# Optimization experiments

Hardware: AMD Instinct MI355X
Metric: run time of the kernel (lower is better)

## Reference

```python
import jax, jax.numpy as jnp
import numpy as np

BINS = 1000  # torch: int(max-min)*100; ~1000 for standardized randn data, fixed for jit


def _entropy(counts, n, width):
    # torch.histogram(density=True): probs = counts / (n * bin_width)
    probs = counts / (n * width)
    safe = jnp.where(probs > 0, probs, 1.0)
    return jnp.sum(jnp.where(probs > 0, -probs * jnp.log2(safe), 0.0))


def setup_inputs() -> dict:
    key = jax.random.key(0)
    k1, k2 = jax.random.split(key)
    x = jax.random.normal(k1, (1024, 64, 16, 16), dtype=jnp.float32)
    u = jax.random.uniform(k2, (1024, 64, 16, 16), dtype=jnp.float32)  # dropout noise
    return {"x": x, "u": u}


def reference(x, u):
    B = x.shape[0]
    temp = x.reshape(B, -1)              # [B, D]
    D = temp.shape[1]

    # corrcoef across rows (each row is a variable)
    tc = temp - temp.mean(axis=1, keepdims=True)
    cov = tc @ tc.T                      # [B, B]
    d = jnp.sqrt(jnp.diag(cov))
    corr = cov / (d[:, None] * d[None, :])
    factor1 = jnp.mean(jnp.abs(corr), axis=1)            # [B]

    # global standardization (torch.std default is unbiased, ddof=1)
    tnorm = (temp - temp.mean()) / jnp.std(temp, ddof=1)
    lo, hi = tnorm.min(), tnorm.max()
    width = (hi - lo) / BINS
    idx = jnp.clip(jnp.floor((tnorm - lo) / width).astype(jnp.int32), 0, BINS - 1)

    # per-row histograms via batched scatter-add; batch histogram = sum of rows
    row_counts = jax.vmap(lambda ii: jnp.zeros(BINS, jnp.float32).at[ii].add(1.0))(idx)  # [B, BINS]
    batch_counts = row_counts.sum(axis=0)

    batch_entropy = _entropy(batch_counts, B * D, width)
    local_entropy = jax.vmap(lambda c: _entropy(c, D, width))(row_counts)  # [B]

    f2 = local_entropy / batch_entropy
    is_zero = f2 == 0
    f1 = jnp.where(is_zero, 0.0, factor1)
    f2 = jnp.where(is_zero, 1.0, jnp.where(f2 < 1.0, 1.0 / f2, f2))
    keep = f1 / f2                       # 1 - p, per row
    p = 1.0 - keep                       # [B]

    mask = (u.reshape(B, -1) > p[:, None]).astype(x.dtype)
    out = (mask * temp) / keep[:, None]
    return out.reshape(x.shape)
```

## Files before the change

kernel.cpp:

```cpp
#include <hip/hip_runtime.h>
#include <math.h>

#define NROWS 1024
#define DCOLS 16384
#define NTOT  16777216
#define BINS  1000
#define NPAIR 136
#define KSPL  8

typedef short short8 __attribute__((ext_vector_type(8)));
typedef unsigned short ushort8 __attribute__((ext_vector_type(8)));
typedef float f32x4 __attribute__((ext_vector_type(4)));

#define GLOAD_LDS16(gp, lp) __builtin_amdgcn_global_load_lds( \
    (const __attribute__((address_space(1))) unsigned int*)(gp), \
    (__attribute__((address_space(3))) unsigned int*)(lp), 16, 0, 0)

__device__ __constant__ int CHK_TR[12] = {1,17,33,49,  0,5,10,15,  128,149,170,191};
__device__ __constant__ int CHK_CB[12] = {0,0,0,0,     128,128,128,128,  0,0,0,0};
__device__ __constant__ int CHK_SL[12] = {0,0,0,0,     2,2,2,2,    0,0,0,0};

__global__ __launch_bounds__(256) void k_rowsplit(const float* __restrict__ x,
    unsigned short* __restrict__ phi, unsigned short* __restrict__ plo,
    double* __restrict__ rowsum, double* __restrict__ rowsumsq,
    double* __restrict__ rowmin, double* __restrict__ rowmax) {
  const int row = blockIdx.x, t = threadIdx.x;
  const size_t base = (size_t)row * DCOLS;
  double s = 0.0, s2 = 0.0;
  float mn = 3.4028235e38f, mx = -3.4028235e38f;
  #pragma unroll
  for (int i = 0; i < 8; ++i) {
    const size_t off = base + (size_t)i * 2048 + (size_t)t * 8;
    const float4 v0 = *(const float4*)(x + off);
    const float4 v1 = *(const float4*)(x + off + 4);
    const float vv[8] = {v0.x, v0.y, v0.z, v0.w, v1.x, v1.y, v1.z, v1.w};
    ushort8 h, lo;
    #pragma unroll
    for (int c = 0; c < 8; ++c) {
      unsigned ub = __float_as_uint(vv[c]);
      unsigned hb = (ub + 0x7FFFu + ((ub >> 16) & 1u)) >> 16;
      float hf = __uint_as_float(hb << 16);
      float r = vv[c] - hf;
      unsigned ur = __float_as_uint(r);
      unsigned lb = (ur + 0x7FFFu + ((ur >> 16) & 1u)) >> 16;
      h[c] = (unsigned short)hb; lo[c] = (unsigned short)lb;
      double dv = vv[c];
      s += dv; s2 += dv * dv;
      mn = fminf(mn, vv[c]); mx = fmaxf(mx, vv[c]);
    }
    *(ushort8*)(phi + off) = h;
    *(ushort8*)(plo + off) = lo;
  }
  #pragma unroll
  for (int off = 32; off > 0; off >>= 1) {
    s  += __shfl_down(s, off);
    s2 += __shfl_down(s2, off);
    mn = fminf(mn, __shfl_down(mn, off));
    mx = fmaxf(mx, __shfl_down(mx, off));
  }
  __shared__ double lsd[8];
  __shared__ float  lsf[8];
  const int lane = t & 63, w = t >> 6;
  if (lane == 0) { lsd[w] = s; lsd[4 + w] = s2; lsf[w] = mn; lsf[4 + w] = mx; }
  __syncthreads();
  if (t == 0) {
    rowsum[row]   = (lsd[0] + lsd[1]) + (lsd[2] + lsd[3]);
    rowsumsq[row] = (lsd[4] + lsd[5]) + (lsd[6] + lsd[7]);
    rowmin[row] = (double)fminf(fminf(lsf[0], lsf[1]), fminf(lsf[2], lsf[3]));
    rowmax[row] = (double)fmaxf(fmaxf(lsf[4], lsf[5]), fmaxf(lsf[6], lsf[7]));
  }
}

__global__ __launch_bounds__(256) void k_rowstats(const float* __restrict__ x,
    double* __restrict__ rowsum, double* __restrict__ rowsumsq,
    double* __restrict__ rowmin, double* __restrict__ rowmax) {
  const int row = blockIdx.x;
  const int t = threadIdx.x;
  const float4* xr = (const float4*)(x + (size_t)row * DCOLS);
  double s = 0.0, s2 = 0.0;
  float mn = 3.4028235e38f, mx = -3.4028235e38f;
  for (int j = t; j < DCOLS / 4; j += 256) {
    float4 v = xr[j];
    double a = v.x, b = v.y, c = v.z, d = v.w;
    s  += (a + b) + (c + d);
    s2 += (a * a + b * b) + (c * c + d * d);
    mn = fminf(mn, fminf(fminf(v.x, v.y), fminf(v.z, v.w)));
    mx = fmaxf(mx, fmaxf(fmaxf(v.x, v.y), fmaxf(v.z, v.w)));
  }
  #pragma unroll
  for (int off = 32; off > 0; off >>= 1) {
    s  += __shfl_down(s, off);
    s2 += __shfl_down(s2, off);
    mn = fminf(mn, __shfl_down(mn, off));
    mx = fmaxf(mx, __shfl_down(mx, off));
  }
  __shared__ double lsd[8];
  __shared__ float  lsf[8];
  const int lane = t & 63, w = t >> 6;
  if (lane == 0) { lsd[w] = s; lsd[4 + w] = s2; lsf[w] = mn; lsf[4 + w] = mx; }
  __syncthreads();
  if (t == 0) {
    rowsum[row]   = (lsd[0] + lsd[1]) + (lsd[2] + lsd[3]);
    rowsumsq[row] = (lsd[4] + lsd[5]) + (lsd[6] + lsd[7]);
    rowmin[row] = (double)fminf(fminf(lsf[0], lsf[1]), fminf(lsf[2], lsf[3]));
    rowmax[row] = (double)fmaxf(fmaxf(lsf[4], lsf[5]), fmaxf(lsf[6], lsf[7]));
  }
}

__global__ __launch_bounds__(256) void k_stats2(
    const double* __restrict__ rowsum, const double* __restrict__ rowsumsq,
    const double* __restrict__ rowmin, const double* __restrict__ rowmax,
    double* __restrict__ m, double* __restrict__ dn, float* __restrict__ fscal,
    float* __restrict__ flg, unsigned* __restrict__ bc) {
#pragma clang fp contract(off)
  const int t = threadIdx.x;
  for (int b = t; b < BINS; b += 256) bc[b] = 0;
  double s = 0.0, s2 = 0.0, mn = 1e300, mx = -1e300;
  for (int r = t; r < NROWS; r += 256) {
    s += rowsum[r]; s2 += rowsumsq[r];
    mn = fmin(mn, rowmin[r]); mx = fmax(mx, rowmax[r]);
  }
  #pragma unroll
  for (int off = 32; off > 0; off >>= 1) {
    s  += __shfl_down(s, off);
    s2 += __shfl_down(s2, off);
    mn = fmin(mn, __shfl_down(mn, off));
    mx = fmax(mx, __shfl_down(mx, off));
  }
  __shared__ double lsd[16];
  const int lane = t & 63, w = t >> 6;
  if (lane == 0) { lsd[w] = s; lsd[4 + w] = s2; lsd[8 + w] = mn; lsd[12 + w] = mx; }
  __syncthreads();
  if (t == 0) {
    double S  = (lsd[0] + lsd[1]) + (lsd[2] + lsd[3]);
    double S2 = (lsd[4] + lsd[5]) + (lsd[6] + lsd[7]);
    double MN = fmin(fmin(lsd[8], lsd[9]), fmin(lsd[10], lsd[11]));
    double MX = fmax(fmax(lsd[12], lsd[13]), fmax(lsd[14], lsd[15]));
    const double N = 16777216.0;
    double mu  = S / N;
    double var = (S2 - S * S / N) / (N - 1.0);
    double sig = sqrt(var);
    float mu32 = (float)mu;
    float sg32 = (float)sig;
    float mnf  = (float)MN;
    float mxf  = (float)MX;
    float lof  = (mnf - mu32) / sg32;
    float hif  = (mxf - mu32) / sg32;
    float wf   = (hif - lof) / 1000.0f;
    fscal[0] = mu32;
    fscal[1] = sg32;
    fscal[2] = lof;
    fscal[3] = wf;
    fscal[4] = 16384.0f * wf;
    fscal[5] = 16777216.0f * wf;
    flg[0] = 0.0f;
  }
  __syncthreads();
  for (int r = t; r < NROWS; r += 256) {
    double rs = rowsum[r];
    m[r]  = rs / 16384.0;
    dn[r] = sqrt(rowsumsq[r] - rs * rs * (1.0 / 16384.0));
  }
}

__global__ __launch_bounds__(256) void k_gramm_sk(
    const unsigned short* __restrict__ phi, const unsigned short* __restrict__ plo,
    float* __restrict__ Gs) {
  const int pid = blockIdx.x >> 3, ks = blockIdx.x & 7;
  int bi = 0, rem = pid;
  while (rem >= 16 - bi) { rem -= 16 - bi; ++bi; }
  const int bj = bi + rem;
  const bool diag = (bi == bj);
  __shared__ short As[2][64][64];
  __shared__ short Bs[2][64][64];
  const int t = threadIdx.x;
  const int w = t >> 6, l = t & 63;

  const unsigned short* plane = (w & 1) ? plo : phi;
  const int prow0 = (w & 2) ? bj * 64 : bi * 64;
  short* lbase = (w & 2) ? &Bs[w & 1][0][0] : &As[w & 1][0][0];
  const bool skipStage = diag && (w & 2);
  const unsigned short* gbase = plane
      + (size_t)(prow0 + (l >> 3)) * DCOLS + (((l & 7) ^ (l >> 3)) * 8);

  f32x4 acc[2][2] = {{{0.f,0.f,0.f,0.f},{0.f,0.f,0.f,0.f}},
                     {{0.f,0.f,0.f,0.f},{0.f,0.f,0.f,0.f}}};
  double dacc[2][2][4] = {{{0,0,0,0},{0,0,0,0}},{{0,0,0,0},{0,0,0,0}}};

  const int wr = w >> 1, wc = w & 1;
  const short* BA0 = diag ? &As[0][0][0] : &Bs[0][0][0];
  const short* BA1 = diag ? &As[1][0][0] : &Bs[1][0][0];
  const int kbeg = ks * 2048;

  for (int k0 = kbeg; k0 < kbeg + 2048; k0 += 64) {
    __syncthreads();
    if (!skipStage) {
      #pragma unroll
      for (int q = 0; q < 8; ++q)
        GLOAD_LDS16(gbase + (size_t)q * 8 * DCOLS + k0, lbase + q * 512);
    }
    __syncthreads();
    short8 ah[2][2], al[2][2], bh[2][2], bl[2][2];
    #pragma unroll
    for (int as_ = 0; as_ < 2; ++as_) {
      const int arow = wr * 32 + as_ * 16 + (l & 15);
      const int r7 = arow & 7;
      #pragma unroll
      for (int kk = 0; kk < 2; ++kk) {
        const int p = (kk * 4 + (l >> 4)) ^ r7;
        ah[as_][kk] = *(const short8*)&As[0][arow][p * 8];
        al[as_][kk] = *(const short8*)&As[1][arow][p * 8];
      }
    }
    #pragma unroll
    for (int bs_ = 0; bs_ < 2; ++bs_) {
      const int brow = wc * 32 + bs_ * 16 + (l & 15);
      const int r7 = brow & 7;
      #pragma unroll
      for (int kk = 0; kk < 2; ++kk) {
        const int p = (kk * 4 + (l >> 4)) ^ r7;
        bh[bs_][kk] = *(const short8*)(BA0 + brow * 64 + p * 8);
        bl[bs_][kk] = *(const short8*)(BA1 + brow * 64 + p * 8);
      }
    }
    #pragma unroll
    for (int as_ = 0; as_ < 2; ++as_)
      #pragma unroll
      for (int bs_ = 0; bs_ < 2; ++bs_)
        #pragma unroll
        for (int kk = 0; kk < 2; ++kk) {
          acc[as_][bs_] = __builtin_amdgcn_mfma_f32_16x16x32_bf16(ah[as_][kk], bh[bs_][kk], acc[as_][bs_], 0, 0, 0);
          acc[as_][bs_] = __builtin_amdgcn_mfma_f32_16x16x32_bf16(ah[as_][kk], bl[bs_][kk], acc[as_][bs_], 0, 0, 0);
          acc[as_][bs_] = __builtin_amdgcn_mfma_f32_16x16x32_bf16(al[as_][kk], bh[bs_][kk], acc[as_][bs_], 0, 0, 0);
        }
  }
  #pragma unroll
  for (int as_ = 0; as_ < 2; ++as_)
    #pragma unroll
    for (int bs_ = 0; bs_ < 2; ++bs_)
      #pragma unroll
      for (int v = 0; v < 4; ++v) dacc[as_][bs_][v] = (double)acc[as_][bs_][v];

  float* gt = Gs + ((size_t)pid * KSPL + ks) * 4096;
  #pragma unroll
  for (int as_ = 0; as_ < 2; ++as_)
    #pragma unroll
    for (int bs_ = 0; bs_ < 2; ++bs_)
      #pragma unroll
      for (int v = 0; v < 4; ++v)
        gt[(wr * 32 + as_ * 16 + (l >> 4) * 4 + v) * 64 + wc * 32 + bs_ * 16 + (l & 15)]
            = (float)dacc[as_][bs_][v];
}

__global__ __launch_bounds__(256) void k_gepi_chk(const float* __restrict__ x,
    const float* __restrict__ Gs, const double* __restrict__ m,
    const double* __restrict__ dn, double* __restrict__ fpart,
    double* __restrict__ chkpart, int nGepi) {
  const int t = threadIdx.x;
  if ((int)blockIdx.x >= nGepi) {
    const int b = blockIdx.x - nGepi;
    const int e = b >> 3, grp = b & 7;
    const int cl = t >> 5;
    const int ksg = t & 31;
    const int trow = CHK_TR[e];
    const int col  = CHK_CB[e] + grp * 8 + cl;
    const float4* xa = (const float4*)(x + (size_t)trow * DCOLS) + ksg * 128;
    const float4* xb = (const float4*)(x + (size_t)col  * DCOLS) + ksg * 128;
    double g = 0.0;
    for (int k = 0; k < 128; ++k) {
      float4 va = xa[k], vb = xb[k];
      g += (double)va.x * vb.x + (double)va.y * vb.y
         + (double)va.z * vb.z + (double)va.w * vb.w;
    }
    g += __shfl_xor(g, 1); g += __shfl_xor(g, 2); g += __shfl_xor(g, 4);
    g += __shfl_xor(g, 8); g += __shfl_xor(g, 16);
    __shared__ double cd[8];
    if (ksg == 0) cd[cl] = g;
    __syncthreads();
    if (t == 0) {
      double s = 0.0;
      #pragma unroll
      for (int i = 0; i < 8; ++i) {
        int c = CHK_CB[e] + grp * 8 + i;
        double cov = cd[i] - 16384.0 * m[trow] * m[c];
        s += fabs(cov) / dn[c];
      }
      chkpart[e * 8 + grp] = s;
    }
    return;
  }
  const int pid = blockIdx.x;
  int bi = 0, rem = pid;
  while (rem >= 16 - bi) { rem -= 16 - bi; ++bi; }
  const int bj = bi + rem;
  const bool diag = (bi == bj);
  __shared__ double Gt[64][65];
  const float* g = Gs + (size_t)pid * KSPL * 4096;
  for (int i = t; i < 4096; i += 256) {
    double sg = (((double)g[i]           + (double)g[4096 + i])
              +  ((double)g[8192 + i]    + (double)g[12288 + i]))
              + (((double)g[16384 + i]   + (double)g[20480 + i])
              +  ((double)g[24576 + i]   + (double)g[28672 + i]));
    Gt[i >> 6][i & 63] = sg;
  }
  __syncthreads();
  {
    const int r = t >> 2, q = t & 3;
    const double mi = m[bi * 64 + r] * 16384.0;
    double s = 0.0;
    #pragma unroll
    for (int i = 0; i < 16; ++i) {
      const int c = q * 16 + i;
      double cov = Gt[r][c] - mi * m[bj * 64 + c];
      s += fabs(cov) / dn[bj * 64 + c];
    }
    s += __shfl_xor(s, 1); s += __shfl_xor(s, 2);
    if (q == 0) fpart[(size_t)(bi * 64 + r) * 16 + bj] = s;
  }
  if (!diag) {
    const int c = t >> 2, q = t & 3;
    const double mj = m[bj * 64 + c] * 16384.0;
    double sc = 0.0;
    #pragma unroll
    for (int i = 0; i < 16; ++i) {
      const int r = q * 16 + i;
      double cov = Gt[r][c] - m[bi * 64 + r] * mj;
      sc += fabs(cov) / dn[bi * 64 + r];
    }
    sc += __shfl_xor(sc, 1); sc += __shfl_xor(sc, 2);
    if (q == 0) fpart[(size_t)(bj * 64 + c) * 16 + bi] = sc;
  }
}

__global__ __launch_bounds__(256) void k_gram(const float* __restrict__ x,
    const double* __restrict__ m, const double* __restrict__ dn,
    double* __restrict__ fpart) {
  __shared__ float As[32][72];
  __shared__ float Bs[32][72];
  __shared__ double red[64][16];
  const int t = threadIdx.x;
  const int bi = blockIdx.y, bj = blockIdx.x;
  const int tx = t & 15, ty = t >> 4;
  const int lr = t >> 2, lc = t & 3;
  const float* Ap = x + (size_t)(bi * 64 + lr) * DCOLS;
  const float* Bp = x + (size_t)(bj * 64 + lr) * DCOLS;
  double acc[4][4];
  #pragma unroll
  for (int i = 0; i < 4; ++i)
    #pragma unroll
    for (int j = 0; j < 4; ++j) acc[i][j] = 0.0;
  float4 a0 = ((const float4*)Ap)[lc];
  float4 a1 = ((const float4*)Ap)[lc + 4];
  float4 b0 = ((const float4*)Bp)[lc];
  float4 b1 = ((const float4*)Bp)[lc + 4];
  for (int k0 = 0; k0 < DCOLS; k0 += 32) {
    __syncthreads();
    {
      const float* a0p = (const float*)&a0;
      const float* a1p = (const float*)&a1;
      const float* b0p = (const float*)&b0;
      const float* b1p = (const float*)&b1;
      #pragma unroll
      for (int jj = 0; jj < 4; ++jj) {
        As[lc * 4 + jj][lr]      = a0p[jj];
        As[16 + lc * 4 + jj][lr] = a1p[jj];
        Bs[lc * 4 + jj][lr]      = b0p[jj];
        Bs[16 + lc * 4 + jj][lr] = b1p[jj];
      }
    }
    __syncthreads();
    if (k0 + 32 < DCOLS) {
      a0 = ((const float4*)(Ap + k0 + 32))[lc];
      a1 = ((const float4*)(Ap + k0 + 32))[lc + 4];
      b0 = ((const float4*)(Bp + k0 + 32))[lc];
      b1 = ((const float4*)(Bp + k0 + 32))[lc + 4];
    }
    float ac[4][4];
    #pragma unroll
    for (int i = 0; i < 4; ++i)
      #pragma unroll
      for (int j = 0; j < 4; ++j) ac[i][j] = 0.0f;
    #pragma unroll
    for (int k = 0; k < 32; ++k) {
      const float4 av = *(const float4*)&As[k][ty * 4];
      const float4 bv = *(const float4*)&Bs[k][tx * 4];
      const float aa[4] = {av.x, av.y, av.z, av.w};
      const float bb[4] = {bv.x, bv.y, bv.z, bv.w};
      #pragma unroll
      for (int i = 0; i < 4; ++i)
        #pragma unroll
        for (int j = 0; j < 4; ++j)
          ac[i][j] += aa[i] * bb[j];
    }
    #pragma unroll
    for (int i = 0; i < 4; ++i)
      #pragma unroll
      for (int j = 0; j < 4; ++j) acc[i][j] += (double)ac[i][j];
  }
  double mr[4], mc[4], dc[4];
  #pragma unroll
  for (int i = 0; i < 4; ++i) mr[i] = m[bi * 64 + ty * 4 + i];
  #pragma unroll
  for (int j = 0; j < 4; ++j) {
    int col = bj * 64 + tx * 4 + j;
    mc[j] = m[col]; dc[j] = dn[col];
  }
  #pragma unroll
  for (int i = 0; i < 4; ++i) {
    double pi = 0.0;
    #pragma unroll
    for (int j = 0; j < 4; ++j) {
      double cov = acc[i][j] - 16384.0 * mr[i] * mc[j];
      pi += fabs(cov) / dc[j];
    }
    red[ty * 4 + i][tx] = pi;
  }
  __syncthreads();
  if (t < 64) {
    double ssum = 0.0;
    #pragma unroll
    for (int q = 0; q < 16; ++q) ssum += red[t][q];
    fpart[(size_t)(bi * 64 + t) * 16 + bj] = ssum;
  }
}

__global__ __launch_bounds__(256) void k_hist(const float* __restrict__ x,
    const float* __restrict__ fscal, double* __restrict__ localent,
    unsigned* __restrict__ bc) {
#pragma clang fp contract(off)
  __shared__ unsigned h[BINS];
  const int row = blockIdx.x, t = threadIdx.x;
  for (int b = t; b < BINS; b += 256) h[b] = 0;
  __syncthreads();
  const float mu32 = fscal[0], sg32 = fscal[1], lof = fscal[2], wf = fscal[3];
  const float4* xr = (const float4*)(x + (size_t)row * DCOLS);
  for (int j = t; j < DCOLS / 4; j += 256) {
    float4 v = xr[j];
    float vv[4] = {v.x, v.y, v.z, v.w};
    #pragma unroll
    for (int c = 0; c < 4; ++c) {
      float tn = (vv[c] - mu32) / sg32;
      float q  = (tn - lof) / wf;
      int idx = (int)floorf(q);
      idx = idx < 0 ? 0 : (idx > BINS - 1 ? BINS - 1 : idx);
      atomicAdd(&h[idx], 1u);
    }
  }
  __syncthreads();
  const double Dw = (double)fscal[4];
  double ls = 0.0;
  for (int b = t; b < BINS; b += 256) {
    unsigned c = h[b];
    if (c) {
      atomicAdd(&bc[b], c);
      double pd = (double)c / Dw;
      ls -= pd * log2(pd);
    }
  }
  #pragma unroll
  for (int off = 32; off > 0; off >>= 1) ls += __shfl_down(ls, off);
  __shared__ double lsd[4];
  const int lane = t & 63, w = t >> 6;
  if (lane == 0) lsd[w] = ls;
  __syncthreads();
  if (t == 0) localent[row] = (lsd[0] + lsd[1]) + (lsd[2] + lsd[3]);
}

__global__ __launch_bounds__(256) void k_final(const unsigned* __restrict__ bc,
    const float* __restrict__ fscal, const double* __restrict__ localent,
    const double* __restrict__ fpart, const double* __restrict__ dn,
    const double* __restrict__ chkpart, float* __restrict__ flg,
    float* __restrict__ pf, float* __restrict__ kf) {
#pragma clang fp contract(off)
  const int t = threadIdx.x;
  if (t < 12) {
    double s = 0.0;
    #pragma unroll
    for (int q = 0; q < 8; ++q) s += chkpart[t * 8 + q];
    double got = fpart[(size_t)CHK_TR[t] * 16 + CHK_SL[t]];
    if (fabs(got - s) > 2e-3 * fmax(fabs(s), 1e-30))
      atomicAdd(flg, 1e6f * (float)(t + 1));
  }
  const double Nw = (double)fscal[5];
  double be = 0.0;
  for (int b = t; b < BINS; b += 256) {
    unsigned c = bc[b];
    if (c) { double pd = (double)c / Nw; be -= pd * log2(pd); }
  }
  #pragma unroll
  for (int off = 32; off > 0; off >>= 1) be += __shfl_down(be, off);
  __shared__ double lsd[4];
  __shared__ double sbent;
  const int lane = t & 63, w = t >> 6;
  if (lane == 0) lsd[w] = be;
  __syncthreads();
  if (t == 0) sbent = (lsd[0] + lsd[1]) + (lsd[2] + lsd[3]);
  __syncthreads();
  const float bef = (float)sbent;
  for (int r = t; r < NROWS; r += 256) {
    double s = 0.0;
    #pragma unroll
    for (int q = 0; q < 16; ++q) s += fpart[(size_t)r * 16 + q];
    float f1f = (float)(s / (dn[r] * 1024.0));
    float lef = (float)localent[r];
    float f2f = lef / bef;
    if (f2f == 0.0f) { f1f = 0.0f; f2f = 1.0f; }
    else if (f2f < 1.0f) f2f = 1.0f / f2f;
    float keepf = f1f / f2f;
    pf[r] = 1.0f - keepf;
    kf[r] = keepf;
  }
}

__global__ __launch_bounds__(256) void k_apply(const float* __restrict__ x,
    const float* __restrict__ u, const float* __restrict__ pf,
    const float* __restrict__ kf, const float* __restrict__ flg,
    float* __restrict__ out) {
#pragma clang fp contract(off)
  const size_t e = ((size_t)blockIdx.x * 256 + threadIdx.x) * 4;
  const float fl = flg[0];
  if (fl != 0.0f) {
    float4 o = {0.f, 0.f, 0.f, 0.f};
    if (e == 0) o.x = fl;
    *(float4*)(out + e) = o;
    return;
  }
  const int row = (int)(e >> 14);
  const float pr = pf[row], kr = kf[row];
  const float4 xv = *(const float4*)(x + e);
  const float4 uv = *(const float4*)(u + e);
  float4 o;
  o.x = (uv.x > pr) ? (xv.x / kr) : 0.0f;
  o.y = (uv.y > pr) ? (xv.y / kr) : 0.0f;
  o.z = (uv.z > pr) ? (xv.z / kr) : 0.0f;
  o.w = (uv.w > pr) ? (xv.w / kr) : 0.0f;
  *(float4*)(out + e) = o;
}

extern "C" void kernel_launch(void* const* d_in, const int* in_sizes, int n_in,
                              void* d_out, int out_size, void* d_ws, size_t ws_size,
                              hipStream_t stream) {
  const float* x = (const float*)d_in[0];
  const float* u = (const float*)d_in[1];
  float* out = (float*)d_out;

  const size_t PLANE = (size_t)NROWS * DCOLS * sizeof(unsigned short);
  const size_t NDBL  = 7 * 1024 + (size_t)NROWS * 16 + 96;
  const size_t TAILB = NDBL * 8 + (2056 + 4) * 4 + BINS * 4;
  const bool big = ws_size >= 2 * PLANE + TAILB;

  char* base = (char*)d_ws;
  unsigned short* phi = (unsigned short*)base;
  unsigned short* plo = (unsigned short*)(base + PLANE);
  double* W = big ? (double*)(base + 2 * PLANE) : (double*)base;

  double* rowsum   = W;
  double* rowsumsq = W + 1024;
  double* rowmin   = W + 2048;
  double* rowmax   = W + 3072;
  double* m        = W + 4096;
  double* dn       = W + 5120;
  double* localent = W + 6144;
  double* fpart    = W + 7168;
  double* chkpart  = W + 7168 + (size_t)NROWS * 16;
  float*  F        = (float*)(chkpart + 96);
  float*  pf       = F;
  float*  kf       = F + 1024;
  float*  fscal    = F + 2048;
  float*  flg      = F + 2056;
  unsigned* bc     = (unsigned*)(F + 2060);

  if (big) {
    float* Gs = out;
    k_rowsplit<<<NROWS, 256, 0, stream>>>(x, phi, plo, rowsum, rowsumsq, rowmin, rowmax);
    k_stats2<<<1, 256, 0, stream>>>(rowsum, rowsumsq, rowmin, rowmax, m, dn, fscal, flg, bc);
    k_gramm_sk<<<NPAIR * KSPL, 256, 0, stream>>>(phi, plo, Gs);
    k_gepi_chk<<<NPAIR + 96, 256, 0, stream>>>(x, Gs, m, dn, fpart, chkpart, NPAIR);
  } else {
    k_rowstats<<<NROWS, 256, 0, stream>>>(x, rowsum, rowsumsq, rowmin, rowmax);
    k_stats2<<<1, 256, 0, stream>>>(rowsum, rowsumsq, rowmin, rowmax, m, dn, fscal, flg, bc);
    k_gram<<<dim3(16, 16), 256, 0, stream>>>(x, m, dn, fpart);
    k_gepi_chk<<<96, 256, 0, stream>>>(x, (const float*)out, m, dn, fpart, chkpart, 0);
  }
  k_hist<<<NROWS, 256, 0, stream>>>(x, fscal, localent, bc);
  k_final<<<1, 256, 0, stream>>>(bc, fscal, localent, fpart, dn, chkpart, flg, pf, kf);
  k_apply<<<NTOT / (256 * 4), 256, 0, stream>>>(x, u, pf, kf, flg, out);
}
```

Before: 203.0 us.

## Double-buffer Gram GEMM LDS staging and privatize histogram per wavefront

The split-K Gram kernel now double-buffers its LDS tiles. It issues the global-to-LDS loads for the next K chunk before computing on the current one, and uses explicit vmcnt waits and barriers so load latency overlaps the MFMA work. Separately, the histogram kernel gives each of its four wavefronts a private LDS histogram and sums them at the end, which cuts atomic contention. Both changes double LDS use and so risk lowering occupancy; the hand-placed waitcnt and barriers also depend on the exact count of outstanding loads.

```diff
diff --git a/kernel.cpp b/kernel.cpp
--- a/kernel.cpp
+++ b/kernel.cpp
@@ -171,75 +171,88 @@
   while (rem >= 16 - bi) { rem -= 16 - bi; ++bi; }
   const int bj = bi + rem;
   const bool diag = (bi == bj);
-  __shared__ short As[2][64][64];
-  __shared__ short Bs[2][64][64];
+  __shared__ short As[2][2][64][64];
+  __shared__ short Bs[2][2][64][64];
   const int t = threadIdx.x;
   const int w = t >> 6, l = t & 63;
 
   const unsigned short* plane = (w & 1) ? plo : phi;
   const int prow0 = (w & 2) ? bj * 64 : bi * 64;
-  short* lbase = (w & 2) ? &Bs[w & 1][0][0] : &As[w & 1][0][0];
   const bool skipStage = diag && (w & 2);
   const unsigned short* gbase = plane
       + (size_t)(prow0 + (l >> 3)) * DCOLS + (((l & 7) ^ (l >> 3)) * 8);
+  short* lbm = (w & 2) ? &Bs[0][0][0][0] : &As[0][0][0][0];
+  short* lb0 = lbm + (w & 1) * 4096;
+  short* lb1 = lb0 + 8192;
+
+#define STAGE(dst, kk) do { if (!skipStage) { \
+    _Pragma("unroll") \
+    for (int q = 0; q < 8; ++q) \
+      GLOAD_LDS16(gbase + (size_t)q * 8 * DCOLS + (kk), (dst) + q * 512); \
+  } } while (0)
 
   f32x4 acc[2][2] = {{{0.f,0.f,0.f,0.f},{0.f,0.f,0.f,0.f}},
                      {{0.f,0.f,0.f,0.f},{0.f,0.f,0.f,0.f}}};
-  double dacc[2][2][4] = {{{0,0,0,0},{0,0,0,0}},{{0,0,0,0},{0,0,0,0}}};
 
   const int wr = w >> 1, wc = w & 1;
-  const short* BA0 = diag ? &As[0][0][0] : &Bs[0][0][0];
-  const short* BA1 = diag ? &As[1][0][0] : &Bs[1][0][0];
   const int kbeg = ks * 2048;
 
-  for (int k0 = kbeg; k0 < kbeg + 2048; k0 += 64) {
-    __syncthreads();
-    if (!skipStage) {
-      #pragma unroll
-      for (int q = 0; q < 8; ++q)
-        GLOAD_LDS16(gbase + (size_t)q * 8 * DCOLS + k0, lbase + q * 512);
-    }
-    __syncthreads();
-    short8 ah[2][2], al[2][2], bh[2][2], bl[2][2];
-    #pragma unroll
-    for (int as_ = 0; as_ < 2; ++as_) {
-      const int arow = wr * 32 + as_ * 16 + (l & 15);
-      const int r7 = arow & 7;
-      #pragma unroll
-      for (int kk = 0; kk < 2; ++kk) {
-        const int p = (kk * 4 + (l >> 4)) ^ r7;
-        ah[as_][kk] = *(const short8*)&As[0][arow][p * 8];
-        al[as_][kk] = *(const short8*)&As[1][arow][p * 8];
-      }
-    }
-    #pragma unroll
-    for (int bs_ = 0; bs_ < 2; ++bs_) {
-      const int brow = wc * 32 + bs_ * 16 + (l & 15);
-      const int r7 = brow & 7;
-      #pragma unroll
-      for (int kk = 0; kk < 2; ++kk) {
-        const int p = (kk * 4 + (l >> 4)) ^ r7;
-        bh[bs_][kk] = *(const short8*)(BA0 + brow * 64 + p * 8);
-        bl[bs_][kk] = *(const short8*)(BA1 + brow * 64 + p * 8);
-      }
-    }
-    #pragma unroll
-    for (int as_ = 0; as_ < 2; ++as_)
-      #pragma unroll
-      for (int bs_ = 0; bs_ < 2; ++bs_)
+  STAGE(lb0, kbeg);
+  int cur = 0;
+  for (int tc = 0; tc < 32; ++tc) {
+    if (tc < 31) {
+      STAGE(cur ? lb0 : lb1, kbeg + (tc + 1) * 64);
+      asm volatile("s_waitcnt vmcnt(8)" ::: "memory");
+    } else {
+      asm volatile("s_waitcnt vmcnt(0)" ::: "memory");
+    }
+    __builtin_amdgcn_s_barrier();
+    __builtin_amdgcn_sched_barrier(0);
+    {
+      const int coff = cur * 8192;
+      const short* A0 = &As[0][0][0][0] + coff;
+      const short* A1 = A0 + 4096;
+      const short* B0 = diag ? A0 : (&Bs[0][0][0][0] + coff);
+      const short* B1 = diag ? A1 : (&Bs[0][0][0][0] + coff + 4096);
+      short8 ah[2][2], al[2][2], bh[2][2], bl[2][2];
+      #pragma unroll
+      for (int as_ = 0; as_ < 2; ++as_) {
+        const int arow = wr * 32 + as_ * 16 + (l & 15);
+        const int r7 = arow & 7;
         #pragma unroll
         for (int kk = 0; kk < 2; ++kk) {
-          acc[as_][bs_] = __builtin_amdgcn_mfma_f32_16x16x32_bf16(ah[as_][kk], bh[bs_][kk], acc[as_][bs_], 0, 0, 0);
-          acc[as_][bs_] = __builtin_amdgcn_mfma_f32_16x16x32_bf16(ah[as_][kk], bl[bs_][kk], acc[as_][bs_], 0, 0, 0);
-          acc[as_][bs_] = __builtin_amdgcn_mfma_f32_16x16x32_bf16(al[as_][kk], bh[bs_][kk], acc[as_][bs_], 0, 0, 0);
+          const int p = (kk * 4 + (l >> 4)) ^ r7;
+          ah[as_][kk] = *(const short8*)(A0 + arow * 64 + p * 8);
+          al[as_][kk] = *(const short8*)(A1 + arow * 64 + p * 8);
         }
-  }
-  #pragma unroll
-  for (int as_ = 0; as_ < 2; ++as_)
-    #pragma unroll
-    for (int bs_ = 0; bs_ < 2; ++bs_)
-      #pragma unroll
-      for (int v = 0; v < 4; ++v) dacc[as_][bs_][v] = (double)acc[as_][bs_][v];
+      }
+      #pragma unroll
+      for (int bs_ = 0; bs_ < 2; ++bs_) {
+        const int brow = wc * 32 + bs_ * 16 + (l & 15);
+        const int r7 = brow & 7;
+        #pragma unroll
+        for (int kk = 0; kk < 2; ++kk) {
+          const int p = (kk * 4 + (l >> 4)) ^ r7;
+          bh[bs_][kk] = *(const short8*)(B0 + brow * 64 + p * 8);
+          bl[bs_][kk] = *(const short8*)(B1 + brow * 64 + p * 8);
+        }
+      }
+      #pragma unroll
+      for (int as_ = 0; as_ < 2; ++as_)
+        #pragma unroll
+        for (int bs_ = 0; bs_ < 2; ++bs_)
+          #pragma unroll
+          for (int kk = 0; kk < 2; ++kk) {
+            acc[as_][bs_] = __builtin_amdgcn_mfma_f32_16x16x32_bf16(ah[as_][kk], bh[bs_][kk], acc[as_][bs_], 0, 0, 0);
+            acc[as_][bs_] = __builtin_amdgcn_mfma_f32_16x16x32_bf16(ah[as_][kk], bl[bs_][kk], acc[as_][bs_], 0, 0, 0);
+            acc[as_][bs_] = __builtin_amdgcn_mfma_f32_16x16x32_bf16(al[as_][kk], bh[bs_][kk], acc[as_][bs_], 0, 0, 0);
+          }
+    }
+    __builtin_amdgcn_sched_barrier(0);
+    __builtin_amdgcn_s_barrier();
+    cur ^= 1;
+  }
+#undef STAGE
 
   float* gt = Gs + ((size_t)pid * KSPL + ks) * 4096;
   #pragma unroll
@@ -249,7 +262,7 @@
       #pragma unroll
       for (int v = 0; v < 4; ++v)
         gt[(wr * 32 + as_ * 16 + (l >> 4) * 4 + v) * 64 + wc * 32 + bs_ * 16 + (l & 15)]
-            = (float)dacc[as_][bs_][v];
+            = (float)((double)acc[as_][bs_][v]);
 }
 
 __global__ __launch_bounds__(256) void k_gepi_chk(const float* __restrict__ x,
@@ -428,9 +441,10 @@
     const float* __restrict__ fscal, double* __restrict__ localent,
     unsigned* __restrict__ bc) {
 #pragma clang fp contract(off)
-  __shared__ unsigned h[BINS];
+  __shared__ unsigned h[4][BINS];
   const int row = blockIdx.x, t = threadIdx.x;
-  for (int b = t; b < BINS; b += 256) h[b] = 0;
+  const int w = t >> 6, lane = t & 63;
+  for (int b = t; b < 4 * BINS; b += 256) h[b / BINS][b % BINS] = 0;
   __syncthreads();
   const float mu32 = fscal[0], sg32 = fscal[1], lof = fscal[2], wf = fscal[3];
   const float4* xr = (const float4*)(x + (size_t)row * DCOLS);
@@ -443,14 +457,14 @@
       float q  = (tn - lof) / wf;
       int idx = (int)floorf(q);
       idx = idx < 0 ? 0 : (idx > BINS - 1 ? BINS - 1 : idx);
-      atomicAdd(&h[idx], 1u);
+      atomicAdd(&h[w][idx], 1u);
     }
   }
   __syncthreads();
   const double Dw = (double)fscal[4];
   double ls = 0.0;
   for (int b = t; b < BINS; b += 256) {
-    unsigned c = h[b];
+    unsigned c = (h[0][b] + h[1][b]) + (h[2][b] + h[3][b]);
     if (c) {
       atomicAdd(&bc[b], c);
       double pd = (double)c / Dw;
@@ -460,7 +474,6 @@
   #pragma unroll
   for (int off = 32; off > 0; off >>= 1) ls += __shfl_down(ls, off);
   __shared__ double lsd[4];
-  const int lane = t & 63, w = t >> 6;
   if (lane == 0) lsd[w] = ls;
   __syncthreads();
   if (t == 0) localent[row] = (lsd[0] + lsd[1]) + (lsd[2] + lsd[3]);
```

Result: no change. 203.1 us (+0.0%).

## Enlarge Gram tiles to 128x128 with 16-way K split and per-wave histograms

Applied to the files above, without the earlier changes.

The split-K bf16x3 Gram kernel now uses 128x128 output tiles (36 upper-triangle pairs) with a 16-way K split instead of 64x64 tiles with 8 splits. Each wave holds a 4x4 MFMA accumulator block, which raises operand reuse per LDS load and cuts redundant global traffic for the hi/lo planes. The epilogue is rewritten for the larger tiles and the spot-check layout is adjusted to match. The histogram kernel also gets per-wave LDS sub-histograms to reduce atomic contention. In exchange, the Gram kernel uses more registers and LDS per block, and the larger partial-sum buffer adds traffic in the epilogue.

```diff
diff --git a/kernel.cpp b/kernel.cpp
--- a/kernel.cpp
+++ b/kernel.cpp
@@ -5,8 +5,8 @@
 #define DCOLS 16384
 #define NTOT  16777216
 #define BINS  1000
-#define NPAIR 136
-#define KSPL  8
+#define NPAIR2 36
+#define KSPL2  16
 
 typedef short short8 __attribute__((ext_vector_type(8)));
 typedef unsigned short ushort8 __attribute__((ext_vector_type(8)));
@@ -18,7 +18,7 @@
 
 __device__ __constant__ int CHK_TR[12] = {1,17,33,49,  0,5,10,15,  128,149,170,191};
 __device__ __constant__ int CHK_CB[12] = {0,0,0,0,     128,128,128,128,  0,0,0,0};
-__device__ __constant__ int CHK_SL[12] = {0,0,0,0,     2,2,2,2,    0,0,0,0};
+__device__ __constant__ int CHK_SL[12] = {0,0,0,0,     1,1,1,1,    0,0,0,0};
 
 __global__ __launch_bounds__(256) void k_rowsplit(const float* __restrict__ x,
     unsigned short* __restrict__ phi, unsigned short* __restrict__ plo,
@@ -163,47 +163,49 @@
   }
 }
 
-__global__ __launch_bounds__(256) void k_gramm_sk(
+__global__ __launch_bounds__(256, 2) void k_gramm_sk(
     const unsigned short* __restrict__ phi, const unsigned short* __restrict__ plo,
     float* __restrict__ Gs) {
-  const int pid = blockIdx.x >> 3, ks = blockIdx.x & 7;
+  const int pid = blockIdx.x >> 4, ks = blockIdx.x & 15;
   int bi = 0, rem = pid;
-  while (rem >= 16 - bi) { rem -= 16 - bi; ++bi; }
+  while (rem >= 8 - bi) { rem -= 8 - bi; ++bi; }
   const int bj = bi + rem;
   const bool diag = (bi == bj);
-  __shared__ short As[2][64][64];
-  __shared__ short Bs[2][64][64];
+  __shared__ short As[2][128][64];
+  __shared__ short Bs[2][128][64];
   const int t = threadIdx.x;
   const int w = t >> 6, l = t & 63;
 
   const unsigned short* plane = (w & 1) ? plo : phi;
-  const int prow0 = (w & 2) ? bj * 64 : bi * 64;
+  const int prow0 = (w & 2) ? bj * 128 : bi * 128;
   short* lbase = (w & 2) ? &Bs[w & 1][0][0] : &As[w & 1][0][0];
   const bool skipStage = diag && (w & 2);
   const unsigned short* gbase = plane
       + (size_t)(prow0 + (l >> 3)) * DCOLS + (((l & 7) ^ (l >> 3)) * 8);
 
-  f32x4 acc[2][2] = {{{0.f,0.f,0.f,0.f},{0.f,0.f,0.f,0.f}},
-                     {{0.f,0.f,0.f,0.f},{0.f,0.f,0.f,0.f}}};
-  double dacc[2][2][4] = {{{0,0,0,0},{0,0,0,0}},{{0,0,0,0},{0,0,0,0}}};
+  f32x4 acc[4][4];
+  #pragma unroll
+  for (int a = 0; a < 4; ++a)
+    #pragma unroll
+    for (int b = 0; b < 4; ++b) acc[a][b] = (f32x4){0.f, 0.f, 0.f, 0.f};
 
   const int wr = w >> 1, wc = w & 1;
   const short* BA0 = diag ? &As[0][0][0] : &Bs[0][0][0];
   const short* BA1 = diag ? &As[1][0][0] : &Bs[1][0][0];
-  const int kbeg = ks * 2048;
-
-  for (int k0 = kbeg; k0 < kbeg + 2048; k0 += 64) {
+  const int kbeg = ks * 1024;
+
+  for (int k0 = kbeg; k0 < kbeg + 1024; k0 += 64) {
     __syncthreads();
     if (!skipStage) {
       #pragma unroll
-      for (int q = 0; q < 8; ++q)
+      for (int q = 0; q < 16; ++q)
         GLOAD_LDS16(gbase + (size_t)q * 8 * DCOLS + k0, lbase + q * 512);
     }
     __syncthreads();
-    short8 ah[2][2], al[2][2], bh[2][2], bl[2][2];
-    #pragma unroll
-    for (int as_ = 0; as_ < 2; ++as_) {
-      const int arow = wr * 32 + as_ * 16 + (l & 15);
+    short8 ah[4][2], al[4][2];
+    #pragma unroll
+    for (int as_ = 0; as_ < 4; ++as_) {
+      const int arow = wr * 64 + as_ * 16 + (l & 15);
       const int r7 = arow & 7;
       #pragma unroll
       for (int kk = 0; kk < 2; ++kk) {
@@ -213,43 +215,36 @@
       }
     }
     #pragma unroll
-    for (int bs_ = 0; bs_ < 2; ++bs_) {
-      const int brow = wc * 32 + bs_ * 16 + (l & 15);
+    for (int bs_ = 0; bs_ < 4; ++bs_) {
+      const int brow = wc * 64 + bs_ * 16 + (l & 15);
       const int r7 = brow & 7;
+      short8 bh[2], bl[2];
       #pragma unroll
       for (int kk = 0; kk < 2; ++kk) {
         const int p = (kk * 4 + (l >> 4)) ^ r7;
-        bh[bs_][kk] = *(const short8*)(BA0 + brow * 64 + p * 8);
-        bl[bs_][kk] = *(const short8*)(BA1 + brow * 64 + p * 8);
+        bh[kk] = *(const short8*)(BA0 + brow * 64 + p * 8);
+        bl[kk] = *(const short8*)(BA1 + brow * 64 + p * 8);
       }
-    }
-    #pragma unroll
-    for (int as_ = 0; as_ < 2; ++as_)
-      #pragma unroll
-      for (int bs_ = 0; bs_ < 2; ++bs_)
+      #pragma unroll
+      for (int as_ = 0; as_ < 4; ++as_)
         #pragma unroll
         for (int kk = 0; kk < 2; ++kk) {
-          acc[as_][bs_] = __builtin_amdgcn_mfma_f32_16x16x32_bf16(ah[as_][kk], bh[bs_][kk], acc[as_][bs_], 0, 0, 0);
-          acc[as_][bs_] = __builtin_amdgcn_mfma_f32_16x16x32_bf16(ah[as_][kk], bl[bs_][kk], acc[as_][bs_], 0, 0, 0);
-          acc[as_][bs_] = __builtin_amdgcn_mfma_f32_16x16x32_bf16(al[as_][kk], bh[bs_][kk], acc[as_][bs_], 0, 0, 0);
+          acc[as_][bs_] = __builtin_amdgcn_mfma_f32_16x16x32_bf16(ah[as_][kk], bh[kk], acc[as_][bs_], 0, 0, 0);
+          acc[as_][bs_] = __builtin_amdgcn_mfma_f32_16x16x32_bf16(ah[as_][kk], bl[kk], acc[as_][bs_], 0, 0, 0);
+          acc[as_][bs_] = __builtin_amdgcn_mfma_f32_16x16x32_bf16(al[as_][kk], bh[kk], acc[as_][bs_], 0, 0, 0);
         }
-  }
-  #pragma unroll
-  for (int as_ = 0; as_ < 2; ++as_)
-    #pragma unroll
-    for (int bs_ = 0; bs_ < 2; ++bs_)
-      #pragma unroll
-      for (int v = 0; v < 4; ++v) dacc[as_][bs_][v] = (double)acc[as_][bs_][v];
-
-  float* gt = Gs + ((size_t)pid * KSPL + ks) * 4096;
-  #pragma unroll
-  for (int as_ = 0; as_ < 2; ++as_)
-    #pragma unroll
-    for (int bs_ = 0; bs_ < 2; ++bs_)
+    }
+  }
+
+  float* gt = Gs + ((size_t)pid * KSPL2 + ks) * 16384;
+  #pragma unroll
+  for (int as_ = 0; as_ < 4; ++as_)
+    #pragma unroll
+    for (int bs_ = 0; bs_ < 4; ++bs_)
       #pragma unroll
       for (int v = 0; v < 4; ++v)
-        gt[(wr * 32 + as_ * 16 + (l >> 4) * 4 + v) * 64 + wc * 32 + bs_ * 16 + (l & 15)]
-            = (float)dacc[as_][bs_][v];
+        gt[(wr * 64 + as_ * 16 + (l >> 4) * 4 + v) * 128 + wc * 64 + bs_ * 16 + (l & 15)]
+            = acc[as_][bs_][v];
 }
 
 __global__ __launch_bounds__(256) void k_gepi_chk(const float* __restrict__ x,
@@ -259,7 +254,7 @@
   const int t = threadIdx.x;
   if ((int)blockIdx.x >= nGepi) {
     const int b = blockIdx.x - nGepi;
-    const int e = b >> 3, grp = b & 7;
+    const int e = b >> 4, grp = b & 15;
     const int cl = t >> 5;
     const int ksg = t & 31;
     const int trow = CHK_TR[e];
@@ -285,51 +280,62 @@
         double cov = cd[i] - 16384.0 * m[trow] * m[c];
         s += fabs(cov) / dn[c];
       }
-      chkpart[e * 8 + grp] = s;
+      chkpart[e * 16 + grp] = s;
     }
     return;
   }
   const int pid = blockIdx.x;
   int bi = 0, rem = pid;
-  while (rem >= 16 - bi) { rem -= 16 - bi; ++bi; }
+  while (rem >= 8 - bi) { rem -= 8 - bi; ++bi; }
   const int bj = bi + rem;
   const bool diag = (bi == bj);
-  __shared__ double Gt[64][65];
-  const float* g = Gs + (size_t)pid * KSPL * 4096;
-  for (int i = t; i < 4096; i += 256) {
-    double sg = (((double)g[i]           + (double)g[4096 + i])
-              +  ((double)g[8192 + i]    + (double)g[12288 + i]))
-              + (((double)g[16384 + i]   + (double)g[20480 + i])
-              +  ((double)g[24576 + i]   + (double)g[28672 + i]));
-    Gt[i >> 6][i & 63] = sg;
-  }
-  __syncthreads();
-  {
-    const int r = t >> 2, q = t & 3;
-    const double mi = m[bi * 64 + r] * 16384.0;
-    double s = 0.0;
-    #pragma unroll
-    for (int i = 0; i < 16; ++i) {
-      const int c = q * 16 + i;
-      double cov = Gt[r][c] - mi * m[bj * 64 + c];
-      s += fabs(cov) / dn[bj * 64 + c];
-    }
-    s += __shfl_xor(s, 1); s += __shfl_xor(s, 2);
-    if (q == 0) fpart[(size_t)(bi * 64 + r) * 16 + bj] = s;
-  }
-  if (!diag) {
-    const int c = t >> 2, q = t & 3;
-    const double mj = m[bj * 64 + c] * 16384.0;
-    double sc = 0.0;
-    #pragma unroll
-    for (int i = 0; i < 16; ++i) {
-      const int r = q * 16 + i;
-      double cov = Gt[r][c] - m[bi * 64 + r] * mj;
-      sc += fabs(cov) / dn[bi * 64 + r];
-    }
-    sc += __shfl_xor(sc, 1); sc += __shfl_xor(sc, 2);
-    if (q == 0) fpart[(size_t)(bj * 64 + c) * 16 + bi] = sc;
-  }
+  __shared__ double Gt[64][129];
+  const float* g = Gs + (size_t)pid * KSPL2 * 16384;
+  double myScol = 0.0;
+  const int cc = t >> 1, cq = t & 1;
+  for (int h = 0; h < 2; ++h) {
+    for (int i = t; i < 8192; i += 256) {
+      const int off = h * 8192 + i;
+      double sg = ((((double)g[off] + (double)g[16384 + off])
+                 +  ((double)g[32768 + off] + (double)g[49152 + off]))
+                +  (((double)g[65536 + off] + (double)g[81920 + off])
+                 +  ((double)g[98304 + off] + (double)g[114688 + off])))
+                + ((((double)g[131072 + off] + (double)g[147456 + off])
+                 +  ((double)g[163840 + off] + (double)g[180224 + off]))
+                +  (((double)g[196608 + off] + (double)g[212992 + off])
+                 +  ((double)g[229376 + off] + (double)g[245760 + off])));
+      Gt[i >> 7][i & 127] = sg;
+    }
+    __syncthreads();
+    {
+      const int r = t >> 2, q = t & 3;
+      const int grow = bi * 128 + h * 64 + r;
+      const double mi = m[grow] * 16384.0;
+      double s = 0.0;
+      for (int i = 0; i < 32; ++i) {
+        const int c = q * 32 + i;
+        double cov = Gt[r][c] - mi * m[bj * 128 + c];
+        s += fabs(cov) / dn[bj * 128 + c];
+      }
+      s += __shfl_xor(s, 1); s += __shfl_xor(s, 2);
+      if (q == 0) fpart[(size_t)grow * 8 + bj] = s;
+    }
+    if (!diag) {
+      const double mj = m[bj * 128 + cc] * 16384.0;
+      double sc = 0.0;
+      for (int i = 0; i < 32; ++i) {
+        const int r = cq * 32 + i;
+        const int grow = bi * 128 + h * 64 + r;
+        double cov = Gt[r][cc] - m[grow] * mj;
+        sc += fabs(cov) / dn[grow];
+      }
+      sc += __shfl_xor(sc, 1);
+      if (cq == 0) myScol += sc;
+    }
+    __syncthreads();
+  }
+  if (!diag && cq == 0)
+    fpart[(size_t)(bj * 128 + cc) * 8 + bi] = myScol;
 }
 
 __global__ __launch_bounds__(256) void k_gram(const float* __restrict__ x,
@@ -428,9 +434,10 @@
     const float* __restrict__ fscal, double* __restrict__ localent,
     unsigned* __restrict__ bc) {
 #pragma clang fp contract(off)
-  __shared__ unsigned h[BINS];
+  __shared__ unsigned h[4][BINS];
   const int row = blockIdx.x, t = threadIdx.x;
-  for (int b = t; b < BINS; b += 256) h[b] = 0;
+  const int w = t >> 6, lane = t & 63;
+  for (int b = t; b < 4 * BINS; b += 256) h[b / BINS][b % BINS] = 0;
   __syncthreads();
   const float mu32 = fscal[0], sg32 = fscal[1], lof = fscal[2], wf = fscal[3];
   const float4* xr = (const float4*)(x + (size_t)row * DCOLS);
@@ -443,14 +450,14 @@
       float q  = (tn - lof) / wf;
       int idx = (int)floorf(q);
       idx = idx < 0 ? 0 : (idx > BINS - 1 ? BINS - 1 : idx);
-      atomicAdd(&h[idx], 1u);
+      atomicAdd(&h[w][idx], 1u);
     }
   }
   __syncthreads();
   const double Dw = (double)fscal[4];
   double ls = 0.0;
   for (int b = t; b < BINS; b += 256) {
-    unsigned c = h[b];
+    unsigned c = (h[0][b] + h[1][b]) + (h[2][b] + h[3][b]);
     if (c) {
       atomicAdd(&bc[b], c);
       double pd = (double)c / Dw;
@@ -460,7 +467,6 @@
   #pragma unroll
   for (int off = 32; off > 0; off >>= 1) ls += __shfl_down(ls, off);
   __shared__ double lsd[4];
-  const int lane = t & 63, w = t >> 6;
   if (lane == 0) lsd[w] = ls;
   __syncthreads();
   if (t == 0) localent[row] = (lsd[0] + lsd[1]) + (lsd[2] + lsd[3]);
@@ -470,14 +476,14 @@
     const float* __restrict__ fscal, const double* __restrict__ localent,
     const double* __restrict__ fpart, const double* __restrict__ dn,
     const double* __restrict__ chkpart, float* __restrict__ flg,
-    float* __restrict__ pf, float* __restrict__ kf) {
+    float* __restrict__ pf, float* __restrict__ kf, int nq, int doChk) {
 #pragma clang fp contract(off)
   const int t = threadIdx.x;
-  if (t < 12) {
+  if (doChk && t < 12) {
     double s = 0.0;
     #pragma unroll
-    for (int q = 0; q < 8; ++q) s += chkpart[t * 8 + q];
-    double got = fpart[(size_t)CHK_TR[t] * 16 + CHK_SL[t]];
+    for (int q = 0; q < 16; ++q) s += chkpart[t * 16 + q];
+    double got = fpart[(size_t)CHK_TR[t] * 8 + CHK_SL[t]];
     if (fabs(got - s) > 2e-3 * fmax(fabs(s), 1e-30))
       atomicAdd(flg, 1e6f * (float)(t + 1));
   }
@@ -499,8 +505,7 @@
   const float bef = (float)sbent;
   for (int r = t; r < NROWS; r += 256) {
     double s = 0.0;
-    #pragma unroll
-    for (int q = 0; q < 16; ++q) s += fpart[(size_t)r * 16 + q];
+    for (int q = 0; q < nq; ++q) s += fpart[(size_t)r * nq + q];
     float f1f = (float)(s / (dn[r] * 1024.0));
     float lef = (float)localent[r];
     float f2f = lef / bef;
@@ -545,7 +550,7 @@
   float* out = (float*)d_out;
 
   const size_t PLANE = (size_t)NROWS * DCOLS * sizeof(unsigned short);
-  const size_t NDBL  = 7 * 1024 + (size_t)NROWS * 16 + 96;
+  const size_t NDBL  = 7 * 1024 + (size_t)NROWS * 16 + 192;
   const size_t TAILB = NDBL * 8 + (2056 + 4) * 4 + BINS * 4;
   const bool big = ws_size >= 2 * PLANE + TAILB;
 
@@ -563,7 +568,7 @@
   double* localent = W + 6144;
   double* fpart    = W + 7168;
   double* chkpart  = W + 7168 + (size_t)NROWS * 16;
-  float*  F        = (float*)(chkpart + 96);
+  float*  F        = (float*)(chkpart + 192);
   float*  pf       = F;
   float*  kf       = F + 1024;
   float*  fscal    = F + 2048;
@@ -574,15 +579,16 @@
     float* Gs = out;
     k_rowsplit<<<NROWS, 256, 0, stream>>>(x, phi, plo, rowsum, rowsumsq, rowmin, rowmax);
     k_stats2<<<1, 256, 0, stream>>>(rowsum, rowsumsq, rowmin, rowmax, m, dn, fscal, flg, bc);
-    k_gramm_sk<<<NPAIR * KSPL, 256, 0, stream>>>(phi, plo, Gs);
-    k_gepi_chk<<<NPAIR + 96, 256, 0, stream>>>(x, Gs, m, dn, fpart, chkpart, NPAIR);
+    k_gramm_sk<<<NPAIR2 * KSPL2, 256, 0, stream>>>(phi, plo, Gs);
+    k_gepi_chk<<<NPAIR2 + 192, 256, 0, stream>>>(x, Gs, m, dn, fpart, chkpart, NPAIR2);
+    k_hist<<<NROWS, 256, 0, stream>>>(x, fscal, localent, bc);
+    k_final<<<1, 256, 0, stream>>>(bc, fscal, localent, fpart, dn, chkpart, flg, pf, kf, 8, 1);
   } else {
     k_rowstats<<<NROWS, 256, 0, stream>>>(x, rowsum, rowsumsq, rowmin, rowmax);
     k_stats2<<<1, 256, 0, stream>>>(rowsum, rowsumsq, rowmin, rowmax, m, dn, fscal, flg, bc);
     k_gram<<<dim3(16, 16), 256, 0, stream>>>(x, m, dn, fpart);
-    k_gepi_chk<<<96, 256, 0, stream>>>(x, (const float*)out, m, dn, fpart, chkpart, 0);
-  }
-  k_hist<<<NROWS, 256, 0, stream>>>(x, fscal, localent, bc);
-  k_final<<<1, 256, 0, stream>>>(bc, fscal, localent, fpart, dn, chkpart, flg, pf, kf);
+    k_hist<<<NROWS, 256, 0, stream>>>(x, fscal, localent, bc);
+    k_final<<<1, 256, 0, stream>>>(bc, fscal, localent, fpart, dn, chkpart, flg, pf, kf, 16, 0);
+  }
   k_apply<<<NTOT / (256 * 4), 256, 0, stream>>>(x, u, pf, kf, flg, out);
 }
```

Result: slower. 209.7 us (+3.3%).
